# Kernel tuning notes

Hardware: AMD Instinct MI355X
Metric: run time of the kernel (lower is better)

Reference implementation:

```python
import jax, jax.numpy as jnp
import numpy as np

B, N, HL, D, HID, O, E, S, K = 8, 64, 32, 256, 1024, 256, 8, 3, 2


def setup_inputs() -> dict:
    key = jax.random.key(0)
    ks = jax.random.split(key, 12)
    w = 0.02
    return {
        "feature_vectors": jax.random.normal(ks[0], (B, N, HL, D), dtype=jnp.float32),
        "object_types": jax.random.uniform(ks[1], (B, N, HL, S, 1), dtype=jnp.float32),
        "gate_w": jax.random.normal(ks[2], (D, E), dtype=jnp.float32) * w,
        "gate_b": jnp.zeros((E,), dtype=jnp.float32),
        "shared_w1": jax.random.normal(ks[3], (S, D, HID), dtype=jnp.float32) * w,
        "shared_b1": jnp.zeros((S, HID), dtype=jnp.float32),
        "shared_w2": jax.random.normal(ks[4], (S, HID, O), dtype=jnp.float32) * w,
        "shared_b2": jnp.zeros((S, O), dtype=jnp.float32),
        "ind_w1": jax.random.normal(ks[5], (E, D, HID), dtype=jnp.float32) * w,
        "ind_b1": jnp.zeros((E, HID), dtype=jnp.float32),
        "ind_w2": jax.random.normal(ks[6], (E, HID, O), dtype=jnp.float32) * w,
        "ind_b2": jnp.zeros((E, O), dtype=jnp.float32),
    }


def reference(feature_vectors, object_types, gate_w, gate_b,
              shared_w1, shared_b1, shared_w2, shared_b2,
              ind_w1, ind_b1, ind_w2, ind_b2):
    b, n, hl, d = feature_vectors.shape
    x = feature_vectors.reshape(-1, d)                      # (T, D)
    T = x.shape[0]

    # gating: softmax -> top-k -> renormalize selected probs
    gates = jax.nn.softmax(x @ gate_w + gate_b, axis=-1)    # (T, E)
    vals, idx = jax.lax.top_k(gates, K)                     # (T, K)
    w = vals / vals.sum(axis=-1, keepdims=True)
    # dense (T, E) combine weights: zero outside top-k, equivalent to scatter-add loop
    w_full = jnp.zeros_like(gates).at[jnp.arange(T)[:, None], idx].set(w)

    # shared experts: all S experts on every token, weighted by object_types
    sh_h = jax.nn.relu(jnp.einsum('td,sdh->tsh', x, shared_w1) + shared_b1)
    sh_o = jnp.einsum('tsh,sho->tso', sh_h, shared_w2) + shared_b2  # (T, S, O)
    obj = object_types.reshape(-1, S, 1)                    # (T, S, 1)
    shared_out = (sh_o * obj).sum(axis=1)                   # (T, O)

    # independent experts: dense all-expert GEMM, combined by masked gate weights
    ih = jax.nn.relu(jnp.einsum('td,edh->teh', x, ind_w1) + ind_b1)
    io = jnp.einsum('teh,eho->teo', ih, ind_w2) + ind_b2    # (T, E, O)
    ind_out = jnp.einsum('te,teo->to', w_full, io)          # (T, O)

    out = 0.5 * shared_out + 0.5 * ind_out
    return out.reshape(b, n, hl, -1)
```

## Files before the change

kernel.cpp:

```cpp
#include <hip/hip_runtime.h>
#include <hip/hip_bf16.h>
#include <stdint.h>

#define TOK   16384
#define DIM   256
#define HIDN  1024
#define OUTD  256
#define NEXP  8
#define NSH   3
#define NSLOT 11
#define TM    64
#define NCH   32

typedef short bf16x8  __attribute__((ext_vector_type(8)));
typedef float f32x4   __attribute__((ext_vector_type(4)));
typedef short short4v __attribute__((ext_vector_type(4)));

constexpr size_t XB_OFF   = 0;
constexpr size_t W1P_OFF  = XB_OFF  + (size_t)TOK*DIM*2;
constexpr size_t W2P_OFF  = W1P_OFF + (size_t)NSLOT*DIM*HIDN*2;
constexpr size_t WTS_OFF  = W2P_OFF + (size_t)NSLOT*HIDN*OUTD*2;
constexpr size_t IDS_OFF  = WTS_OFF + (size_t)TOK*2*4;
constexpr size_t CNT_OFF  = IDS_OFF + (size_t)TOK*2*4;
constexpr size_t LTOK_OFF = CNT_OFF + 256;
constexpr size_t LW_OFF   = LTOK_OFF + (size_t)NEXP*TOK*4;
constexpr size_t WS_NEED  = LW_OFF + (size_t)NEXP*TOK*4;

__device__ __forceinline__ unsigned short f2bf(float f) {
    __hip_bfloat16 h = __float2bfloat16(f);
    return *reinterpret_cast<unsigned short*>(&h);
}

__device__ __forceinline__ f32x4 mfma16(bf16x8 a, bf16x8 b, f32x4 c) {
    return __builtin_amdgcn_mfma_f32_16x16x32_bf16(a, b, c, 0, 0, 0);
}

__device__ __forceinline__ void gload_lds16(const void* g, void* l) {
    __builtin_amdgcn_global_load_lds(
        (const __attribute__((address_space(1))) unsigned int*)g,
        (__attribute__((address_space(3))) unsigned int*)l, 16, 0, 0);
}

__device__ __forceinline__ int hoff(int row, int colb) {
    return (row << 6) + ((colb + ((row & 7) << 4)) & 63);
}

__device__ __forceinline__ void fence_sched() { __builtin_amdgcn_sched_barrier(0); }

__global__ __launch_bounds__(256) void k_prep(
    const float* __restrict__ x, const float* __restrict__ gw,
    const float* __restrict__ gb, short* __restrict__ xb,
    float* __restrict__ wts, int* __restrict__ ids) {
    int wid = threadIdx.x >> 6, lane = threadIdx.x & 63;
    int t = blockIdx.x * 4 + wid;
    const float* xr = x + (size_t)t * DIM;
    {
        float4 v = reinterpret_cast<const float4*>(xr)[lane];
        short4v o;
        o[0] = (short)f2bf(v.x); o[1] = (short)f2bf(v.y);
        o[2] = (short)f2bf(v.z); o[3] = (short)f2bf(v.w);
        reinterpret_cast<short4v*>(xb + (size_t)t * DIM)[lane] = o;
    }
    float acc[NEXP] = {0.f,0.f,0.f,0.f,0.f,0.f,0.f,0.f};
    #pragma unroll
    for (int i = 0; i < DIM/64; ++i) {
        int d = i*64 + lane;
        float xv = xr[d];
        const float* g = gw + (size_t)d * NEXP;
        #pragma unroll
        for (int e = 0; e < NEXP; ++e) acc[e] = fmaf(xv, g[e], acc[e]);
    }
    #pragma unroll
    for (int off = 32; off; off >>= 1) {
        #pragma unroll
        for (int e = 0; e < NEXP; ++e) acc[e] += __shfl_xor(acc[e], off, 64);
    }
    if (lane == 0) {
        float l[NEXP];
        #pragma unroll
        for (int e = 0; e < NEXP; ++e) l[e] = acc[e] + gb[e];
        int e0 = 0; float v0 = l[0];
        #pragma unroll
        for (int e = 1; e < NEXP; ++e) if (l[e] > v0) { v0 = l[e]; e0 = e; }
        int e1 = -1; float v1 = -1e30f;
        #pragma unroll
        for (int e = 0; e < NEXP; ++e) if (e != e0 && l[e] > v1) { v1 = l[e]; e1 = e; }
        float r = expf(v1 - v0);
        float w0 = 0.5f / (1.f + r);
        float w1 = 0.5f * r / (1.f + r);
        ids[2*t]   = e0;  ids[2*t+1] = e1;
        wts[2*t]   = w0;  wts[2*t+1] = w1;
    }
}

__global__ __launch_bounds__(256) void k_convert_w(
    const float* __restrict__ sw1, const float* __restrict__ iw1,
    const float* __restrict__ sw2, const float* __restrict__ iw2,
    short* __restrict__ w1p, short* __restrict__ w2p) {
    __shared__ float tile[32][68];
    int bid = blockIdx.x, tid = threadIdx.x;
    const int W1B = NSLOT * 8 * 16;
    bool isW1 = bid < W1B;
    int b = isW1 ? bid : bid - W1B;
    int NTG = isW1 ? 16 : 4;
    int KT  = isW1 ? 8 : 32;
    int NT  = isW1 ? 64 : 16;
    int Nd  = isW1 ? HIDN : OUTD;
    int ntg = b % NTG; b /= NTG;
    int kt  = b % KT;
    int slot = b / KT;
    const float* src;
    if (isW1) src = (slot < NSH) ? sw1 + (size_t)slot*DIM*HIDN  : iw1 + (size_t)(slot-NSH)*DIM*HIDN;
    else      src = (slot < NSH) ? sw2 + (size_t)slot*HIDN*OUTD : iw2 + (size_t)(slot-NSH)*HIDN*OUTD;
    {
        int tr = tid >> 3, tc = (tid & 7) * 8;
        const float* s = src + (size_t)(kt*32 + tr)*Nd + ntg*64 + tc;
        float4 v0 = *reinterpret_cast<const float4*>(s);
        float4 v1 = *reinterpret_cast<const float4*>(s + 4);
        *reinterpret_cast<float4*>(&tile[tr][tc])     = v0;
        *reinterpret_cast<float4*>(&tile[tr][tc + 4]) = v1;
    }
    __syncthreads();
    {
        int ntl = tid >> 6, lane = tid & 63;
        int n  = ntl*16 + (lane & 15);
        int k8 = (lane >> 4) * 8;
        bf16x8 o;
        #pragma unroll
        for (int j = 0; j < 8; ++j) o[j] = (short)f2bf(tile[k8 + j][n]);
        size_t gidx = (((size_t)slot*KT + kt)*NT + ntg*4 + ntl)*64 + lane;
        short* dst = isW1 ? w1p : w2p;
        reinterpret_cast<bf16x8*>(dst)[gidx] = o;
    }
}

__global__ __launch_bounds__(256) void k_route(
    const int* __restrict__ ids, const float* __restrict__ wts,
    int* __restrict__ cnt, int* __restrict__ ltok, float* __restrict__ lw) {
    __shared__ int lcnt[NEXP];
    __shared__ int gbase[NEXP];
    int tid = threadIdx.x;
    if (tid < NEXP) lcnt[tid] = 0;
    __syncthreads();
    int t = blockIdx.x * 256 + tid;
    int e0 = ids[2*t], e1 = ids[2*t+1];
    int p0 = atomicAdd(&lcnt[e0], 1);
    int p1 = atomicAdd(&lcnt[e1], 1);
    __syncthreads();
    if (tid < NEXP) gbase[tid] = atomicAdd(&cnt[tid], lcnt[tid]);
    __syncthreads();
    size_t o0 = (size_t)e0*TOK + gbase[e0] + p0;
    size_t o1 = (size_t)e1*TOK + gbase[e1] + p1;
    ltok[o0] = t;  lw[o0] = wts[2*t];
    ltok[o1] = t;  lw[o1] = wts[2*t+1];
}

__global__ __launch_bounds__(512) void k_moe(
    const short* __restrict__ xb, const short* __restrict__ w1p, const short* __restrict__ w2p,
    const float* __restrict__ sb1, const float* __restrict__ sb2,
    const float* __restrict__ ib1, const float* __restrict__ ib2,
    const float* __restrict__ obj, const int* __restrict__ cnt,
    const int* __restrict__ ltok, const float* __restrict__ lw,
    float* __restrict__ out)
{
    __shared__ __align__(16) char Xs[32768];
    __shared__ __align__(16) char Wb1[16384];
    __shared__ __align__(16) char Wb2[16384];
    __shared__ __align__(16) char Hs[4096];
    __shared__ float bias_lds[HIDN];
    __shared__ int   tokl[TM];
    __shared__ float twl[TM];

    const int slot = blockIdx.y;
    const int m0   = blockIdx.x * TM;
    const bool sh  = slot < NSH;
    const int e    = slot - NSH;
    int count = TOK;
    if (!sh) { count = cnt[e]; if (m0 >= count) return; }

    const int tid  = threadIdx.x;
    const int w    = tid >> 6, lane = tid & 63;
    const int wm   = w >> 1,   wn   = w & 1;
    const int pm   = w >> 2,   pn   = w & 3;
    const int lrow = lane & 15, g   = lane >> 4;

    if (tid < TM) {
        if (sh) {
            tokl[tid] = m0 + tid;
            twl[tid]  = 0.5f * obj[(size_t)(m0 + tid)*NSH + slot];
        } else {
            int p = m0 + tid;
            bool ok = p < count;
            tokl[tid] = ok ? ltok[(size_t)e*TOK + p] : 0;
            twl[tid]  = ok ? lw[(size_t)e*TOK + p] : 0.f;
        }
    }
    __syncthreads();

    const char* w1base = (const char*)w1p;
    const char* w2base = (const char*)w2p;
    const float* b1v = sh ? (sb1 + slot*HIDN) : (ib1 + (size_t)e*HIDN);

    {
        #pragma unroll
        for (int i = 0; i < 4; ++i) {
            int idx = w*4 + i;
            int kt = idx >> 2, mt = idx & 3;
            const short* src = xb + (size_t)tokl[mt*16 + lrow]*DIM + kt*32 + g*8;
            gload_lds16(src, Xs + (idx << 10));
        }
        if (w < 4)
            gload_lds16((const char*)b1v + w*1024 + lane*16, (char*)bias_lds + w*1024);
    }
    auto stage_w1 = [&](int c) {
        #pragma unroll
        for (int i = 0; i < 2; ++i)
            gload_lds16(
                w1base + ((((size_t)slot*8 + w)*64 + c*2 + i) << 10) + lane*16,
                Wb1 + ((w*2 + i) << 10));
    };
    auto stage_w2 = [&](int c) {
        const char* s2 = w2base + ((((size_t)slot*32 + c)*16) << 10);
        #pragma unroll
        for (int i = 0; i < 2; ++i)
            gload_lds16(s2 + ((w*2 + i) << 10) + lane*16, Wb2 + ((w*2 + i) << 10));
    };
    stage_w1(0);
    stage_w2(0);
    __syncthreads();

    f32x4 acc2[2][4] = {};
    for (int c = 0; c < NCH; ++c) {
        if (c > 0) stage_w2(c);
        fence_sched();
        asm volatile("s_waitcnt vmcnt(2)" ::: "memory");
        fence_sched();
        __builtin_amdgcn_s_barrier();
        fence_sched();

        f32x4 acc1 = {};
        #pragma unroll
        for (int kt = 0; kt < 8; ++kt) {
            bf16x8 a = *reinterpret_cast<const bf16x8*>(
                Xs + ((kt*4 + wm) << 10) + lane*16);
            bf16x8 b = *reinterpret_cast<const bf16x8*>(
                Wb1 + ((kt*2 + wn) << 10) + lane*16);
            acc1 = mfma16(a, b, acc1);
        }
        {
            int col = wn*16 + lrow;
            float bias = bias_lds[c*32 + col];
            #pragma unroll
            for (int r = 0; r < 4; ++r) {
                int row = wm*16 + g*4 + r;
                float v = fmaxf(acc1[r] + bias, 0.f) * twl[row];
                *reinterpret_cast<unsigned short*>(Hs + hoff(row, col*2)) = f2bf(v);
            }
        }
        fence_sched();
        asm volatile("s_waitcnt lgkmcnt(0)" ::: "memory");
        fence_sched();
        __builtin_amdgcn_s_barrier();
        fence_sched();

        if (c + 1 < NCH) stage_w1(c + 1);
        fence_sched();
        if (c + 1 < NCH) { asm volatile("s_waitcnt vmcnt(2)" ::: "memory"); }
        else             { asm volatile("s_waitcnt vmcnt(0)" ::: "memory"); }
        fence_sched();
        __builtin_amdgcn_s_barrier();
        fence_sched();

        {
            bf16x8 a2[2];
            #pragma unroll
            for (int mf = 0; mf < 2; ++mf)
                a2[mf] = *reinterpret_cast<const bf16x8*>(
                    Hs + hoff(pm*32 + mf*16 + lrow, g*16));
            #pragma unroll
            for (int nf = 0; nf < 4; ++nf) {
                bf16x8 b2 = *reinterpret_cast<const bf16x8*>(
                    Wb2 + ((pn*4 + nf) << 10) + lane*16);
                #pragma unroll
                for (int mf = 0; mf < 2; ++mf)
                    acc2[mf][nf] = mfma16(a2[mf], b2, acc2[mf][nf]);
            }
        }
        fence_sched();
        __builtin_amdgcn_s_barrier();
        fence_sched();
    }

    {
        const float* b2 = sh ? (sb2 + slot*OUTD) : (ib2 + (size_t)e*OUTD);
        #pragma unroll
        for (int mf = 0; mf < 2; ++mf)
            #pragma unroll
            for (int nf = 0; nf < 4; ++nf) {
                int col = pn*64 + nf*16 + lrow;
                #pragma unroll
                for (int r = 0; r < 4; ++r) {
                    int row = pm*32 + mf*16 + g*4 + r;
                    if (sh || (m0 + row < count)) {
                        int t = tokl[row];
                        float v = acc2[mf][nf][r] + twl[row] * b2[col];
                        atomicAdd(&out[(size_t)t*OUTD + col], v);
                    }
                }
            }
    }
}

extern "C" void kernel_launch(void* const* d_in, const int* in_sizes, int n_in,
                              void* d_out, int out_size, void* d_ws, size_t ws_size,
                              hipStream_t stream) {
    const float* x   = (const float*)d_in[0];
    const float* obj = (const float*)d_in[1];
    const float* gw  = (const float*)d_in[2];
    const float* gb  = (const float*)d_in[3];
    const float* sw1 = (const float*)d_in[4];
    const float* sb1 = (const float*)d_in[5];
    const float* sw2 = (const float*)d_in[6];
    const float* sb2 = (const float*)d_in[7];
    const float* iw1 = (const float*)d_in[8];
    const float* ib1 = (const float*)d_in[9];
    const float* iw2 = (const float*)d_in[10];
    const float* ib2 = (const float*)d_in[11];
    float* out = (float*)d_out;
    char* ws = (char*)d_ws;
    if (ws_size < WS_NEED) return;

    short* xb   = (short*)(ws + XB_OFF);
    short* w1p  = (short*)(ws + W1P_OFF);
    short* w2p  = (short*)(ws + W2P_OFF);
    float* wts  = (float*)(ws + WTS_OFF);
    int*   ids  = (int*)  (ws + IDS_OFF);
    int*   cnt  = (int*)  (ws + CNT_OFF);
    int*   ltok = (int*)  (ws + LTOK_OFF);
    float* lwt  = (float*)(ws + LW_OFF);

    hipMemsetAsync(ws + CNT_OFF, 0, 256, stream);
    hipMemsetAsync(out, 0, (size_t)out_size * 4, stream);
    k_prep<<<TOK/4, 256, 0, stream>>>(x, gw, gb, xb, wts, ids);
    k_convert_w<<<NSLOT*8*16 + NSLOT*32*4, 256, 0, stream>>>(sw1, iw1, sw2, iw2, w1p, w2p);
    k_route<<<TOK/256, 256, 0, stream>>>(ids, wts, cnt, ltok, lwt);
    k_moe<<<dim3(TOK/TM, NSLOT), 512, 0, stream>>>(
        xb, w1p, w2p, sb1, sb2, ib1, ib2, obj, cnt, ltok, lwt, out);
}
```

Before: 211.1 us.

## Warp-specialize MoE kernel into GEMM1 producer and GEMM2 consumer waves

Splits the eight waves into four producers that compute the first GEMM (relu hidden chunk) and four consumers that compute the second GEMM one chunk behind, with double-buffered W1/W2/H tiles in LDS and one barrier per step. Producers now read X activations directly from global memory instead of staging them in LDS. The H swizzle is changed to a different rotation. This aims to overlap the two GEMM phases and cut the number of barriers per chunk. In exchange, each wave does half the MFMA work in its phase, it relies on global/L2 latency for the X operand, and consumers carry more accumulators, which raises register pressure.

```diff
diff --git a/kernel.cpp b/kernel.cpp
--- a/kernel.cpp
+++ b/kernel.cpp
@@ -41,11 +41,10 @@
         (__attribute__((address_space(3))) unsigned int*)l, 16, 0, 0);
 }
 
-__device__ __forceinline__ int hoff(int row, int colb) {
-    return (row << 6) + ((colb + ((row & 7) << 4)) & 63);
-}
-
-__device__ __forceinline__ void fence_sched() { __builtin_amdgcn_sched_barrier(0); }
+__device__ __forceinline__ int hoff(int row, int cb) {
+    int rot = ((row >> 1) + (row >> 2)) & 3;
+    return (row << 6) + ((((cb >> 4) + rot) & 3) << 4) + (cb & 15);
+}
 
 __global__ __launch_bounds__(256) void k_prep(
     const float* __restrict__ x, const float* __restrict__ gw,
@@ -163,10 +162,9 @@
     const int* __restrict__ ltok, const float* __restrict__ lw,
     float* __restrict__ out)
 {
-    __shared__ __align__(16) char Xs[32768];
-    __shared__ __align__(16) char Wb1[16384];
-    __shared__ __align__(16) char Wb2[16384];
-    __shared__ __align__(16) char Hs[4096];
+    __shared__ __align__(16) char Wb1[2][16384];
+    __shared__ __align__(16) char Wb2[2][16384];
+    __shared__ __align__(16) char Hs[2][4096];
     __shared__ float bias_lds[HIDN];
     __shared__ int   tokl[TM];
     __shared__ float twl[TM];
@@ -180,9 +178,11 @@
 
     const int tid  = threadIdx.x;
     const int w    = tid >> 6, lane = tid & 63;
-    const int wm   = w >> 1,   wn   = w & 1;
-    const int pm   = w >> 2,   pn   = w & 3;
     const int lrow = lane & 15, g   = lane >> 4;
+    const bool producer = w < 4;
+    const int m2  = (w >> 1) & 1;
+    const int n16 = w & 1;
+    const int cw  = w - 4;
 
     if (tid < TM) {
         if (sh) {
@@ -201,106 +201,99 @@
     const char* w2base = (const char*)w2p;
     const float* b1v = sh ? (sb1 + slot*HIDN) : (ib1 + (size_t)e*HIDN);
 
-    {
+    int tokA0 = tokl[m2*32 + 0*16 + lrow];
+    int tokA1 = tokl[m2*32 + 1*16 + lrow];
+
+    auto stage_w1 = [&](int c) {
         #pragma unroll
         for (int i = 0; i < 4; ++i) {
             int idx = w*4 + i;
-            int kt = idx >> 2, mt = idx & 3;
-            const short* src = xb + (size_t)tokl[mt*16 + lrow]*DIM + kt*32 + g*8;
-            gload_lds16(src, Xs + (idx << 10));
+            gload_lds16(
+                w1base + ((((size_t)slot*8 + (idx >> 1))*64 + c*2 + (idx & 1)) << 10) + lane*16,
+                Wb1[c & 1] + (idx << 10));
         }
-        if (w < 4)
-            gload_lds16((const char*)b1v + w*1024 + lane*16, (char*)bias_lds + w*1024);
-    }
-    auto stage_w1 = [&](int c) {
-        #pragma unroll
-        for (int i = 0; i < 2; ++i)
-            gload_lds16(
-                w1base + ((((size_t)slot*8 + w)*64 + c*2 + i) << 10) + lane*16,
-                Wb1 + ((w*2 + i) << 10));
     };
     auto stage_w2 = [&](int c) {
         const char* s2 = w2base + ((((size_t)slot*32 + c)*16) << 10);
         #pragma unroll
-        for (int i = 0; i < 2; ++i)
-            gload_lds16(s2 + ((w*2 + i) << 10) + lane*16, Wb2 + ((w*2 + i) << 10));
+        for (int i = 0; i < 4; ++i) {
+            int idx = cw*4 + i;
+            gload_lds16(s2 + (idx << 10) + lane*16, Wb2[c & 1] + (idx << 10));
+        }
     };
-    stage_w1(0);
-    stage_w2(0);
-    __syncthreads();
-
-    f32x4 acc2[2][4] = {};
-    for (int c = 0; c < NCH; ++c) {
-        if (c > 0) stage_w2(c);
-        fence_sched();
-        asm volatile("s_waitcnt vmcnt(2)" ::: "memory");
-        fence_sched();
-        __builtin_amdgcn_s_barrier();
-        fence_sched();
-
-        f32x4 acc1 = {};
-        #pragma unroll
-        for (int kt = 0; kt < 8; ++kt) {
-            bf16x8 a = *reinterpret_cast<const bf16x8*>(
-                Xs + ((kt*4 + wm) << 10) + lane*16);
-            bf16x8 b = *reinterpret_cast<const bf16x8*>(
-                Wb1 + ((kt*2 + wn) << 10) + lane*16);
-            acc1 = mfma16(a, b, acc1);
-        }
-        {
-            int col = wn*16 + lrow;
-            float bias = bias_lds[c*32 + col];
-            #pragma unroll
-            for (int r = 0; r < 4; ++r) {
-                int row = wm*16 + g*4 + r;
-                float v = fmaxf(acc1[r] + bias, 0.f) * twl[row];
-                *reinterpret_cast<unsigned short*>(Hs + hoff(row, col*2)) = f2bf(v);
+
+    if (producer) stage_w1(0);
+    else {
+        gload_lds16((const char*)b1v + cw*1024 + lane*16,
+                    (char*)bias_lds + cw*1024);
+    }
+    __syncthreads();
+
+    f32x4 acc2[4][4] = {};
+    for (int s = 0; s <= NCH; ++s) {
+        if (producer) {
+            if (s < NCH) {
+                if (s + 1 < NCH) stage_w1(s + 1);
+                asm volatile("" : "+v"(tokA0), "+v"(tokA1));
+                const char* wb = Wb1[s & 1];
+                f32x4 acc1[2] = {};
+                #pragma unroll
+                for (int kt = 0; kt < 8; ++kt) {
+                    bf16x8 a0 = *reinterpret_cast<const bf16x8*>(
+                        xb + (size_t)tokA0*DIM + kt*32 + g*8);
+                    bf16x8 a1 = *reinterpret_cast<const bf16x8*>(
+                        xb + (size_t)tokA1*DIM + kt*32 + g*8);
+                    bf16x8 b = *reinterpret_cast<const bf16x8*>(
+                        wb + ((kt*2 + n16) << 10) + lane*16);
+                    acc1[0] = mfma16(a0, b, acc1[0]);
+                    acc1[1] = mfma16(a1, b, acc1[1]);
+                }
+                char* hb = Hs[s & 1];
+                int col = n16*16 + lrow;
+                float bias = bias_lds[s*32 + col];
+                #pragma unroll
+                for (int mf = 0; mf < 2; ++mf)
+                    #pragma unroll
+                    for (int r = 0; r < 4; ++r) {
+                        int row = m2*32 + mf*16 + g*4 + r;
+                        float v = fmaxf(acc1[mf][r] + bias, 0.f) * twl[row];
+                        *reinterpret_cast<unsigned short*>(hb + hoff(row, col*2)) = f2bf(v);
+                    }
+            }
+        } else {
+            if (s < NCH) stage_w2(s);
+            if (s >= 1) {
+                const int d = s - 1;
+                const char* hb = Hs[d & 1];
+                const char* wb = Wb2[d & 1];
+                bf16x8 a2[4];
+                #pragma unroll
+                for (int mf = 0; mf < 4; ++mf)
+                    a2[mf] = *reinterpret_cast<const bf16x8*>(
+                        hb + hoff(mf*16 + lrow, g*16));
+                #pragma unroll
+                for (int nf = 0; nf < 4; ++nf) {
+                    bf16x8 b2 = *reinterpret_cast<const bf16x8*>(
+                        wb + ((cw*4 + nf) << 10) + lane*16);
+                    #pragma unroll
+                    for (int mf = 0; mf < 4; ++mf)
+                        acc2[mf][nf] = mfma16(a2[mf], b2, acc2[mf][nf]);
+                }
             }
         }
-        fence_sched();
-        asm volatile("s_waitcnt lgkmcnt(0)" ::: "memory");
-        fence_sched();
-        __builtin_amdgcn_s_barrier();
-        fence_sched();
-
-        if (c + 1 < NCH) stage_w1(c + 1);
-        fence_sched();
-        if (c + 1 < NCH) { asm volatile("s_waitcnt vmcnt(2)" ::: "memory"); }
-        else             { asm volatile("s_waitcnt vmcnt(0)" ::: "memory"); }
-        fence_sched();
-        __builtin_amdgcn_s_barrier();
-        fence_sched();
-
-        {
-            bf16x8 a2[2];
-            #pragma unroll
-            for (int mf = 0; mf < 2; ++mf)
-                a2[mf] = *reinterpret_cast<const bf16x8*>(
-                    Hs + hoff(pm*32 + mf*16 + lrow, g*16));
+        __syncthreads();
+    }
+
+    if (!producer) {
+        const float* b2 = sh ? (sb2 + slot*OUTD) : (ib2 + (size_t)e*OUTD);
+        #pragma unroll
+        for (int mf = 0; mf < 4; ++mf)
             #pragma unroll
             for (int nf = 0; nf < 4; ++nf) {
-                bf16x8 b2 = *reinterpret_cast<const bf16x8*>(
-                    Wb2 + ((pn*4 + nf) << 10) + lane*16);
-                #pragma unroll
-                for (int mf = 0; mf < 2; ++mf)
-                    acc2[mf][nf] = mfma16(a2[mf], b2, acc2[mf][nf]);
-            }
-        }
-        fence_sched();
-        __builtin_amdgcn_s_barrier();
-        fence_sched();
-    }
-
-    {
-        const float* b2 = sh ? (sb2 + slot*OUTD) : (ib2 + (size_t)e*OUTD);
-        #pragma unroll
-        for (int mf = 0; mf < 2; ++mf)
-            #pragma unroll
-            for (int nf = 0; nf < 4; ++nf) {
-                int col = pn*64 + nf*16 + lrow;
+                int col = cw*64 + nf*16 + lrow;
                 #pragma unroll
                 for (int r = 0; r < 4; ++r) {
-                    int row = pm*32 + mf*16 + g*4 + r;
+                    int row = mf*16 + g*4 + r;
                     if (sh || (m0 + row < count)) {
                         int t = tokl[row];
                         float v = acc2[mf][nf][r] + twl[row] * b2[col];
```

Result: slower. 553.5 us (+162.2%).
